# Kernel tuning notes

Measured on AMD Instinct MI355X. Metric: run time of the kernel, lower is better.

## Reference

```python
import jax, jax.numpy as jnp
import numpy as np

B_, S_, P_, D_ = 2, 512, 64, 1024
L_ = 4            # n_layer
DI_ = 2 * D_      # d_inner (expand=2)
DS_ = 16          # d_state
DC_ = 4           # d_conv
DR_ = D_ // 16    # dt_rank
PCD_ = 768        # prepend_cond_dim


def setup_inputs() -> dict:
    key = jax.random.key(0)
    ks = jax.random.split(key, 12)
    n = lambda k, s, sc=0.02: jax.random.normal(k, s, dtype=jnp.float32) * sc
    A_log = jnp.log(jnp.broadcast_to(jnp.arange(1, DS_ + 1, dtype=jnp.float32), (L_, DI_, DS_)))
    return {
        'x': jax.random.normal(ks[0], (B_, S_, D_), dtype=jnp.float32),
        'prepend_cond': jax.random.normal(ks[1], (B_, P_, PCD_), dtype=jnp.float32),
        'pre_w1': n(ks[2], (PCD_, D_)),
        'pre_w2': n(ks[3], (D_, D_)),
        'norm_w': jnp.ones((L_, D_), jnp.float32),
        'in_proj_w': n(ks[4], (L_, 2 * DI_, D_)),
        'conv_w': n(ks[5], (L_, DI_, DC_), 0.1),
        'conv_b': jnp.zeros((L_, DI_), jnp.float32),
        'x_proj_w': n(ks[6], (L_, DR_ + 2 * DS_, DI_)),
        'dt_proj_w': n(ks[7], (L_, DI_, DR_), 0.1),
        'dt_proj_b': jax.random.uniform(ks[8], (L_, DI_), jnp.float32, -4.0, -2.0),
        'A_log': A_log,
        'D_param': jnp.ones((L_, DI_), jnp.float32),
        'out_proj_w': n(ks[9], (L_, D_, DI_)),
        'final_norm_w': jnp.ones((D_,), jnp.float32),
    }


def rmsnorm(x, w, eps=1e-5):
    return x * jax.lax.rsqrt(jnp.mean(x * x, axis=-1, keepdims=True) + eps) * w


def mamba_block(x, ip_w, cw, cb, xp_w, dtp_w, dtp_b, A_log, Dp, op_w):
    B, S, _ = x.shape
    xz = jnp.einsum('bsd,ed->bse', x, ip_w)            # [B,S,2*DI]
    xi, z = jnp.split(xz, 2, axis=-1)
    # depthwise causal conv1d along time
    xt = xi.transpose(0, 2, 1)                          # [B,DI,S]
    conv = jax.lax.conv_general_dilated(
        xt, cw[:, None, :], (1,), [(DC_ - 1, 0)], feature_group_count=DI_) + cb[:, None]
    xi = jax.nn.silu(conv.transpose(0, 2, 1))           # [B,S,DI]
    xdbl = jnp.einsum('bse,fe->bsf', xi, xp_w)          # [B,S,DR+2*DS]
    dt, Bm, Cm = jnp.split(xdbl, [DR_, DR_ + DS_], axis=-1)
    dt = jax.nn.softplus(jnp.einsum('bsr,er->bse', dt, dtp_w) + dtp_b)  # [B,S,DI]
    A = -jnp.exp(A_log)                                 # [DI,DS]
    dA = jnp.exp(dt[..., None] * A)                     # [B,S,DI,DS]
    dBu = dt[..., None] * Bm[:, :, None, :] * xi[..., None]

    def step(h, t):
        da, dbu, c = t
        h = da * h + dbu                                # [B,DI,DS]
        return h, jnp.einsum('bes,bs->be', h, c)

    h0 = jnp.zeros((B, DI_, DS_), x.dtype)
    _, ys = jax.lax.scan(step, h0, (dA.transpose(1, 0, 2, 3), dBu.transpose(1, 0, 2, 3), Cm.transpose(1, 0, 2)))
    y = ys.transpose(1, 0, 2) + xi * Dp
    y = y * jax.nn.silu(z)
    return jnp.einsum('bse,de->bsd', y, op_w)


def reference(x, prepend_cond, pre_w1, pre_w2, norm_w, in_proj_w, conv_w, conv_b,
              x_proj_w, dt_proj_w, dt_proj_b, A_log, D_param, out_proj_w, final_norm_w):
    p = jax.nn.silu(prepend_cond @ pre_w1) @ pre_w2     # to_prepend_embed
    h = jnp.concatenate([p, x], axis=1)                 # [B, P+S, D]
    for l in range(L_):
        h = h + mamba_block(rmsnorm(h, norm_w[l]), in_proj_w[l], conv_w[l], conv_b[l],
                            x_proj_w[l], dt_proj_w[l], dt_proj_b[l], A_log[l],
                            D_param[l], out_proj_w[l])
    h = rmsnorm(h, final_norm_w)
    return h[:, P_:, :]
```

## Files before the change

kernel.cpp:

```cpp
#include <hip/hip_runtime.h>
#include <math.h>

#define B_ 2
#define S_ 512
#define P_ 64
#define T_ 576
#define D_ 1024
#define L_ 4
#define DI_ 2048
#define DS_ 16
#define DC_ 4
#define DR_ 64
#define PCD_ 768
#define M_ (B_*T_)
#define CCH 18
#define NC (T_/CCH)
#define XKS 16

typedef __attribute__((ext_vector_type(8))) short bf16x8;
typedef __attribute__((ext_vector_type(4))) float f32x4;

__device__ __forceinline__ float silu_f(float v) { return v / (1.f + __expf(-v)); }
__device__ __forceinline__ float softplus_f(float v) {
    return fmaxf(v, 0.f) + log1pf(__expf(-fabsf(v)));
}
__device__ __forceinline__ unsigned short bf16_rne(float x) {
    unsigned int b = __float_as_uint(x);
    b += 0x7fffu + ((b >> 16) & 1u);
    return (unsigned short)(b >> 16);
}
__device__ __forceinline__ float bf16_to_f(unsigned short u) {
    return __uint_as_float((unsigned int)u << 16);
}

typedef const void __attribute__((address_space(1)))* gas_t;
typedef void __attribute__((address_space(3)))* las_t;
__device__ __forceinline__ void async16(const void* g, void* l) {
    __builtin_amdgcn_global_load_lds((gas_t)g, (las_t)l, 16, 0, 0);
}

template<int EPI>
__global__ __launch_bounds__(256) void gemm_mfma_kernel(
    const unsigned short* __restrict__ A, const unsigned short* __restrict__ W,
    float* __restrict__ C, const float* __restrict__ bias,
    int M, int N, int K, int Kchunk)
{
    __shared__ unsigned short As[128 * 32];
    __shared__ unsigned short Bs[128 * 32];
    const int tid = threadIdx.x;
    const int wave = tid >> 6;
    const int lane = tid & 63;
    const int m0 = blockIdx.y * 128, n0 = blockIdx.x * 128;
    const int kbase = blockIdx.z * Kchunk;
    const int wm = (wave >> 1) * 64, wn = (wave & 1) * 64;

    const int srow = (wave << 5) + (lane >> 2);
    const int selem = (lane & 3) * 8;
    const unsigned short* gA = A + (size_t)(m0 + srow) * K + kbase + selem;
    const unsigned short* gB = W + (size_t)(n0 + srow) * K + kbase + selem;
    unsigned short* lA = As + (wave << 5) * 32;
    unsigned short* lB = Bs + (wave << 5) * 32;

    f32x4 acc[4][4];
    #pragma unroll
    for (int i = 0; i < 4; ++i)
        #pragma unroll
        for (int j = 0; j < 4; ++j)
            acc[i][j] = (f32x4){0.f, 0.f, 0.f, 0.f};

    const int fr = lane & 15;
    const int fq = lane >> 4;
    const int aoff = (wm + fr) * 32 + fq * 8;
    const int boff = (wn + fr) * 32 + fq * 8;

    for (int k0 = 0; k0 < Kchunk; k0 += 32) {
        async16(gA, lA);
        async16(gA + (size_t)16 * K, lA + 16 * 32);
        async16(gB, lB);
        async16(gB + (size_t)16 * K, lB + 16 * 32);
        gA += 32; gB += 32;
        __syncthreads();
        bf16x8 af[4], bf[4];
        #pragma unroll
        for (int i = 0; i < 4; ++i) af[i] = *(const bf16x8*)&As[aoff + i * 512];
        #pragma unroll
        for (int j = 0; j < 4; ++j) bf[j] = *(const bf16x8*)&Bs[boff + j * 512];
        #pragma unroll
        for (int i = 0; i < 4; ++i)
            #pragma unroll
            for (int j = 0; j < 4; ++j)
                acc[i][j] = __builtin_amdgcn_mfma_f32_16x16x32_bf16(
                    af[i], bf[j], acc[i][j], 0, 0, 0);
        __syncthreads();
    }

    #pragma unroll
    for (int i = 0; i < 4; ++i) {
        const int m = m0 + wm + i * 16 + fq * 4;
        #pragma unroll
        for (int j = 0; j < 4; ++j) {
            const int n = n0 + wn + j * 16 + fr;
            if (EPI == 6) {
                float* p = C + ((size_t)blockIdx.z * M + m) * N + n;
                #pragma unroll
                for (int r = 0; r < 4; ++r)
                    p[(size_t)r * N] = acc[i][j][r];
            } else {
                float* p = C + (size_t)m * N + n;
                #pragma unroll
                for (int r = 0; r < 4; ++r)
                    p[(size_t)r * N] = acc[i][j][r];
            }
        }
    }
}

__global__ __launch_bounds__(256) void dtproj_kernel(
    const unsigned short* __restrict__ dtr,
    const unsigned short* __restrict__ Wb,
    const float* __restrict__ bias,
    float* __restrict__ dtb)
{
    __shared__ float As[16][DR_];
    const int tid = threadIdx.x;
    const int e = blockIdx.x * 256 + tid;
    const int m0 = blockIdx.y * 16;
    {
        const ushort4 a4 = ((const ushort4*)(dtr + (size_t)m0 * DR_))[tid];
        float* dst = &As[0][0] + tid * 4;
        dst[0] = bf16_to_f(a4.x);
        dst[1] = bf16_to_f(a4.y);
        dst[2] = bf16_to_f(a4.z);
        dst[3] = bf16_to_f(a4.w);
    }
    float w[DR_];
    {
        const ushort4* wp = (const ushort4*)(Wb + (size_t)e * DR_);
        #pragma unroll
        for (int q = 0; q < 16; ++q) {
            const ushort4 v = wp[q];
            w[q * 4 + 0] = bf16_to_f(v.x);
            w[q * 4 + 1] = bf16_to_f(v.y);
            w[q * 4 + 2] = bf16_to_f(v.z);
            w[q * 4 + 3] = bf16_to_f(v.w);
        }
    }
    __syncthreads();
    const float bb = bias[e];
    #pragma unroll
    for (int m = 0; m < 16; ++m) {
        float acc = 0.f;
        #pragma unroll
        for (int r = 0; r < DR_; ++r) acc = fmaf(As[m][r], w[r], acc);
        dtb[(size_t)(m0 + m) * DI_ + e] = softplus_f(acc + bb);
    }
}

__global__ __launch_bounds__(256) void xproj_mfma_kernel(
    const unsigned short* __restrict__ A,
    const unsigned short* __restrict__ W,
    float* __restrict__ P)
{
    __shared__ unsigned short As[128 * 32];
    __shared__ unsigned short Bs[96 * 32];
    const int tid = threadIdx.x;
    const int wave = tid >> 6;
    const int lane = tid & 63;
    const int m0 = blockIdx.y * 128;
    const int kbase = blockIdx.x * (DI_ / XKS);
    const int wm = (wave >> 1) * 64, wn = (wave & 1) * 48;

    const int srow = (wave << 5) + (lane >> 2);
    const int selem = (lane & 3) * 8;
    const unsigned short* gA = A + (size_t)(m0 + srow) * DI_ + kbase + selem;
    const unsigned short* gB = W + (size_t)srow * DI_ + kbase + selem;
    unsigned short* lA = As + (wave << 5) * 32;
    unsigned short* lB = Bs + (wave << 5) * 32;

    f32x4 acc[4][3];
    #pragma unroll
    for (int i = 0; i < 4; ++i)
        #pragma unroll
        for (int j = 0; j < 3; ++j)
            acc[i][j] = (f32x4){0.f, 0.f, 0.f, 0.f};

    const int fr = lane & 15;
    const int fq = lane >> 4;
    const int aoff = (wm + fr) * 32 + fq * 8;
    const int boff = (wn + fr) * 32 + fq * 8;

    #pragma unroll
    for (int kk = 0; kk < 4; ++kk) {
        async16(gA, lA);
        async16(gA + (size_t)16 * DI_, lA + 16 * 32);
        if (wave < 3) {
            async16(gB, lB);
            async16(gB + (size_t)16 * DI_, lB + 16 * 32);
        }
        gA += 32; gB += 32;
        __syncthreads();
        bf16x8 af[4], bf[3];
        #pragma unroll
        for (int i = 0; i < 4; ++i) af[i] = *(const bf16x8*)&As[aoff + i * 512];
        #pragma unroll
        for (int j = 0; j < 3; ++j) bf[j] = *(const bf16x8*)&Bs[boff + j * 512];
        #pragma unroll
        for (int i = 0; i < 4; ++i)
            #pragma unroll
            for (int j = 0; j < 3; ++j)
                acc[i][j] = __builtin_amdgcn_mfma_f32_16x16x32_bf16(
                    af[i], bf[j], acc[i][j], 0, 0, 0);
        __syncthreads();
    }

    float* Pb = P + ((size_t)blockIdx.x * M_ + m0) * 96;
    #pragma unroll
    for (int i = 0; i < 4; ++i) {
        const int m = wm + i * 16 + fq * 4;
        #pragma unroll
        for (int j = 0; j < 3; ++j) {
            const int n = wn + j * 16 + fr;
            #pragma unroll
            for (int r = 0; r < 4; ++r)
                Pb[(size_t)(m + r) * 96 + n] = acc[i][j][r];
        }
    }
}

__global__ __launch_bounds__(256) void xproj_reduce_kernel(
    const float* __restrict__ P, float* __restrict__ Bc, float* __restrict__ Cc,
    unsigned short* __restrict__ dtr_bf)
{
    const int i = blockIdx.x * 256 + threadIdx.x;
    if (i >= M_ * 96) return;
    float s = 0.f;
    #pragma unroll
    for (int ks = 0; ks < XKS; ++ks) s += P[(size_t)ks * (M_ * 96) + i];
    const int m = i / 96;
    const int n = i - m * 96;
    if (n < DR_)            dtr_bf[(size_t)m * DR_ + n] = bf16_rne(s);
    else if (n < DR_ + DS_) Bc[(size_t)m * DS_ + (n - DR_)] = s;
    else                    Cc[(size_t)m * DS_ + (n - DR_ - DS_)] = s;
}

__global__ __launch_bounds__(256) void cvt_bf16_kernel(
    const float* __restrict__ in, unsigned short* __restrict__ out, int n4)
{
    const int i = blockIdx.x * 256 + threadIdx.x;
    if (i >= n4) return;
    const float4 v = ((const float4*)in)[i];
    ushort4 o;
    o.x = bf16_rne(v.x); o.y = bf16_rne(v.y);
    o.z = bf16_rne(v.z); o.w = bf16_rne(v.w);
    ((ushort4*)out)[i] = o;
}

__global__ __launch_bounds__(256) void cvt3_kernel(
    const float* __restrict__ s0, unsigned short* __restrict__ d0, int n0,
    const float* __restrict__ s1, unsigned short* __restrict__ d1, int n1,
    const float* __restrict__ s2, unsigned short* __restrict__ d2, int n2)
{
    const int i = blockIdx.x * 256 + threadIdx.x;
    const float* s; unsigned short* d; int off;
    if (i < n0)           { s = s0; d = d0; off = i; }
    else if (i < n0 + n1) { s = s1; d = d1; off = i - n0; }
    else if (i < n0 + n1 + n2) { s = s2; d = d2; off = i - n0 - n1; }
    else return;
    const float4 v = ((const float4*)s)[off];
    ushort4 o;
    o.x = bf16_rne(v.x); o.y = bf16_rne(v.y);
    o.z = bf16_rne(v.z); o.w = bf16_rne(v.w);
    ((ushort4*)d)[off] = o;
}

__global__ __launch_bounds__(256) void cvt_transpose_kernel(
    const float* __restrict__ in, unsigned short* __restrict__ out, int K, int N)
{
    __shared__ float t[64][65];
    const int k0 = blockIdx.x * 64;
    const int n0 = blockIdx.y * 64;
    const int tx = threadIdx.x & 63;
    const int ty = threadIdx.x >> 6;
    #pragma unroll
    for (int j = 0; j < 16; ++j) {
        const int kk = ty * 16 + j;
        t[kk][tx] = in[(size_t)(k0 + kk) * N + n0 + tx];
    }
    __syncthreads();
    #pragma unroll
    for (int j = 0; j < 16; ++j) {
        const int nn = ty * 16 + j;
        out[(size_t)(n0 + nn) * K + k0 + tx] = bf16_rne(t[tx][nn]);
    }
}

__global__ __launch_bounds__(256) void reduce_silu_bf16_kernel(
    const float* __restrict__ P, unsigned short* __restrict__ o, int MN, int ns)
{
    const int i = blockIdx.x * 256 + threadIdx.x;
    if (i >= MN) return;
    float s = 0.f;
    for (int k = 0; k < ns; ++k) s += P[(size_t)k * MN + i];
    o[i] = bf16_rne(silu_f(s));
}
__global__ __launch_bounds__(256) void reduce_fp32_kernel(
    const float* __restrict__ P, float* __restrict__ o, int MN, int ns)
{
    const int i = blockIdx.x * 256 + threadIdx.x;
    if (i >= MN) return;
    float s = 0.f;
    for (int k = 0; k < ns; ++k) s += P[(size_t)k * MN + i];
    o[i] = s;
}

__global__ __launch_bounds__(256) void outproj_reduce_kernel(
    const float* __restrict__ P, float* __restrict__ h)
{
    const int i = blockIdx.x * 256 + threadIdx.x;
    const float4 a = ((const float4*)P)[i];
    const float4 b = ((const float4*)P)[i + M_ * D_ / 4];
    float4 hv = ((float4*)h)[i];
    hv.x += a.x + b.x; hv.y += a.y + b.y;
    hv.z += a.z + b.z; hv.w += a.w + b.w;
    ((float4*)h)[i] = hv;
}

__global__ __launch_bounds__(256) void assemble_h_kernel(
    const float* __restrict__ p, const float* __restrict__ x, float* __restrict__ h)
{
    const int idx = blockIdx.x * 256 + threadIdx.x;
    const int r = idx >> 8;
    const int c = idx & 255;
    const int b = r / T_;
    const int t = r - b * T_;
    float4 v;
    if (t < P_) v = ((const float4*)p)[(size_t)(b * P_ + t) * 256 + c];
    else        v = ((const float4*)x)[(size_t)(b * S_ + (t - P_)) * 256 + c];
    ((float4*)h)[idx] = v;
}

__global__ __launch_bounds__(256) void rmsnorm_bf16_kernel(
    const float* __restrict__ x, const float* __restrict__ w,
    unsigned short* __restrict__ outb)
{
    const int r = blockIdx.x;
    const float4 v = ((const float4*)(x + (size_t)r * D_))[threadIdx.x];
    float ss = v.x * v.x + v.y * v.y + v.z * v.z + v.w * v.w;
    ss += __shfl_xor(ss, 32, 64);
    ss += __shfl_xor(ss, 16, 64);
    ss += __shfl_xor(ss, 8, 64);
    ss += __shfl_xor(ss, 4, 64);
    ss += __shfl_xor(ss, 2, 64);
    ss += __shfl_xor(ss, 1, 64);
    __shared__ float red[4];
    if ((threadIdx.x & 63) == 0) red[threadIdx.x >> 6] = ss;
    __syncthreads();
    const float tot = red[0] + red[1] + red[2] + red[3];
    const float scale = rsqrtf(tot * (1.f / D_) + 1e-5f);
    const float4 wv = ((const float4*)w)[threadIdx.x];
    ushort4 o;
    o.x = bf16_rne(v.x * scale * wv.x);
    o.y = bf16_rne(v.y * scale * wv.y);
    o.z = bf16_rne(v.z * scale * wv.z);
    o.w = bf16_rne(v.w * scale * wv.w);
    ((ushort4*)(outb + (size_t)r * D_))[threadIdx.x] = o;
}

__global__ __launch_bounds__(256) void final_rmsnorm_kernel(
    const float* __restrict__ h, const float* __restrict__ w, float* __restrict__ out)
{
    const int r = blockIdx.x;
    const int b = r / S_;
    const int s = r - b * S_;
    const int hr = b * T_ + P_ + s;
    const float4 v = ((const float4*)(h + (size_t)hr * D_))[threadIdx.x];
    float ss = v.x * v.x + v.y * v.y + v.z * v.z + v.w * v.w;
    ss += __shfl_xor(ss, 32, 64);
    ss += __shfl_xor(ss, 16, 64);
    ss += __shfl_xor(ss, 8, 64);
    ss += __shfl_xor(ss, 4, 64);
    ss += __shfl_xor(ss, 2, 64);
    ss += __shfl_xor(ss, 1, 64);
    __shared__ float red[4];
    if ((threadIdx.x & 63) == 0) red[threadIdx.x >> 6] = ss;
    __syncthreads();
    const float tot = red[0] + red[1] + red[2] + red[3];
    const float scale = rsqrtf(tot * (1.f / D_) + 1e-5f);
    const float4 wv = ((const float4*)w)[threadIdx.x];
    float4 o;
    o.x = v.x * scale * wv.x; o.y = v.y * scale * wv.y;
    o.z = v.z * scale * wv.z; o.w = v.w * scale * wv.w;
    ((float4*)(out + (size_t)r * D_))[threadIdx.x] = o;
}

__global__ __launch_bounds__(256) void conv_silu_kernel(
    const float* __restrict__ xz, const float* __restrict__ cw,
    const float* __restrict__ cb, unsigned short* __restrict__ xib,
    float* __restrict__ xim, float* __restrict__ szm)
{
    __shared__ float xs[67][64];
    const int tid = threadIdx.x;
    const int tx = tid & 63;
    const int ty = tid >> 6;
    const int r0 = blockIdx.x * 64;
    const int e0 = blockIdx.y * 64;
    const int bt0 = (r0 / T_) * T_;

    for (int j = ty; j < 67; j += 4) {
        const int r = r0 + j - 3;
        xs[j][tx] = (r >= bt0) ? xz[(size_t)r * (2 * DI_) + e0 + tx] : 0.f;
    }
    __syncthreads();
    const float4 w = *(const float4*)(cw + (size_t)(e0 + tx) * 4);
    const float bias = cb[e0 + tx];
    #pragma unroll
    for (int j = 0; j < 16; ++j) {
        const int rl = ty * 16 + j;
        float v = bias;
        v = fmaf(w.x, xs[rl + 0][tx], v);
        v = fmaf(w.y, xs[rl + 1][tx], v);
        v = fmaf(w.z, xs[rl + 2][tx], v);
        v = fmaf(w.w, xs[rl + 3][tx], v);
        const float o = silu_f(v);
        const size_t go = (size_t)(r0 + rl) * DI_ + e0 + tx;
        xib[go] = bf16_rne(o);
        xim[go] = o;
        szm[go] = silu_f(xz[(size_t)(r0 + rl) * (2 * DI_) + DI_ + e0 + tx]);
    }
}

__global__ __launch_bounds__(256) void scan_chunk1_kernel(
    const float* __restrict__ dtm,
    const float* __restrict__ Bc,
    const float* __restrict__ xim,
    const float* __restrict__ A_log,
    float* __restrict__ Ap, float* __restrict__ Hp)
{
    __shared__ float4 Bs[CCH][4];
    const int tid = threadIdx.x;
    const int e = ((blockIdx.x & 7) << 8) + tid;
    const int cb = blockIdx.x >> 3;
    const int b = cb & (B_ - 1);
    const int c = cb >> 1;
    const int r0 = b * T_ + c * CCH;
    for (int i = tid; i < CCH * DS_; i += 256)
        ((float*)Bs)[i] = Bc[(size_t)r0 * DS_ + i];
    float A2[DS_], h[DS_], a[DS_];
    const float* Ae = A_log + (size_t)e * DS_;
    #pragma unroll
    for (int s = 0; s < DS_; ++s) {
        A2[s] = -__expf(Ae[s]) * 1.44269504f;
        h[s] = 0.f; a[s] = 1.f;
    }
    __syncthreads();
    const float* dp = dtm + (size_t)r0 * DI_ + e;
    const float* up = xim + (size_t)r0 * DI_ + e;
    #pragma unroll
    for (int t = 0; t < CCH; ++t) {
        const float dtv = dp[(size_t)t * DI_];
        const float dtu = dtv * up[(size_t)t * DI_];
        #pragma unroll
        for (int q = 0; q < 4; ++q) {
            const float4 bq = Bs[t][q];
            const float* bb = &bq.x;
            #pragma unroll
            for (int j = 0; j < 4; ++j) {
                const int s = q * 4 + j;
                const float da = __builtin_amdgcn_exp2f(dtv * A2[s]);
                a[s] *= da;
                h[s] = fmaf(da, h[s], bb[j] * dtu);
            }
        }
    }
    const size_t o = (size_t)cb * DS_ * DI_ + e;
    #pragma unroll
    for (int s = 0; s < DS_; ++s) {
        Ap[o + (size_t)s * DI_] = a[s];
        Hp[o + (size_t)s * DI_] = h[s];
    }
}

__global__ __launch_bounds__(256) void scan_chunk2_kernel(
    float* __restrict__ Ap, float* __restrict__ Hp)
{
    const int g = blockIdx.x * 256 + threadIdx.x;
    float h = 0.f;
    #pragma unroll
    for (int c = 0; c < NC; ++c) {
        const size_t o = (size_t)c * (B_ * DI_ * DS_) + g;
        const float ap = Ap[o];
        const float hp = Hp[o];
        Hp[o] = h;
        h = fmaf(ap, h, hp);
    }
}

__global__ __launch_bounds__(256) void scan_chunk3_kernel(
    const float* __restrict__ dtm,
    const float* __restrict__ Bc,
    const float* __restrict__ Cc,
    const float* __restrict__ xim,
    const float* __restrict__ szm,
    const float* __restrict__ A_log, const float* __restrict__ Dp,
    const float* __restrict__ Hin, unsigned short* __restrict__ y)
{
    __shared__ float4 Bs[CCH][4], Cs[CCH][4];
    const int tid = threadIdx.x;
    const int e = ((blockIdx.x & 7) << 8) + tid;
    const int cb = blockIdx.x >> 3;
    const int b = cb & (B_ - 1);
    const int c = cb >> 1;
    const int r0 = b * T_ + c * CCH;
    for (int i = tid; i < CCH * DS_; i += 256) {
        ((float*)Bs)[i] = Bc[(size_t)r0 * DS_ + i];
        ((float*)Cs)[i] = Cc[(size_t)r0 * DS_ + i];
    }
    float A2[DS_], h[DS_];
    const float* Ae = A_log + (size_t)e * DS_;
    const float dpe = Dp[e];
    const size_t ho = (size_t)cb * DS_ * DI_ + e;
    #pragma unroll
    for (int s = 0; s < DS_; ++s) {
        A2[s] = -__expf(Ae[s]) * 1.44269504f;
        h[s] = Hin[ho + (size_t)s * DI_];
    }
    __syncthreads();
    const float* dp = dtm + (size_t)r0 * DI_ + e;
    const float* up = xim + (size_t)r0 * DI_ + e;
    const float* sp = szm + (size_t)r0 * DI_ + e;
    unsigned short* yp = y + (size_t)r0 * DI_ + e;
    #pragma unroll
    for (int t = 0; t < CCH; ++t) {
        const float dtv = dp[(size_t)t * DI_];
        const float u   = up[(size_t)t * DI_];
        const float dtu = dtv * u;
        float y0 = 0.f, y1 = 0.f, y2 = 0.f, y3 = 0.f;
        #pragma unroll
        for (int q = 0; q < 4; ++q) {
            const float4 bq = Bs[t][q];
            const float4 cq = Cs[t][q];
            const float* bb = &bq.x;
            const float* cc = &cq.x;
            #pragma unroll
            for (int j = 0; j < 4; ++j) {
                const int s = q * 4 + j;
                const float da = __builtin_amdgcn_exp2f(dtv * A2[s]);
                h[s] = fmaf(da, h[s], bb[j] * dtu);
                if (j == 0)      y0 = fmaf(h[s], cc[j], y0);
                else if (j == 1) y1 = fmaf(h[s], cc[j], y1);
                else if (j == 2) y2 = fmaf(h[s], cc[j], y2);
                else             y3 = fmaf(h[s], cc[j], y3);
            }
        }
        const float ysum = (y0 + y1) + (y2 + y3);
        const float yv = fmaf(u, dpe, ysum) * sp[(size_t)t * DI_];
        yp[(size_t)t * DI_] = bf16_rne(yv);
    }
}

extern "C" void kernel_launch(void* const* d_in, const int* in_sizes, int n_in,
                              void* d_out, int out_size, void* d_ws, size_t ws_size,
                              hipStream_t stream)
{
    const float* x       = (const float*)d_in[0];
    const float* pc      = (const float*)d_in[1];
    const float* pre_w1  = (const float*)d_in[2];
    const float* pre_w2  = (const float*)d_in[3];
    const float* norm_w  = (const float*)d_in[4];
    const float* ip_w    = (const float*)d_in[5];
    const float* conv_w  = (const float*)d_in[6];
    const float* conv_b  = (const float*)d_in[7];
    const float* xp_w    = (const float*)d_in[8];
    const float* dtp_w   = (const float*)d_in[9];
    const float* dtp_b   = (const float*)d_in[10];
    const float* A_log   = (const float*)d_in[11];
    const float* D_param = (const float*)d_in[12];
    const float* op_w    = (const float*)d_in[13];
    const float* fnw     = (const float*)d_in[14];
    float* out = (float*)d_out;

    float* ws = (float*)d_ws;
    float* h    = ws;  ws += (size_t)M_ * D_;
    float* xz   = ws;  ws += (size_t)M_ * 2 * DI_;
    float* xim  = ws;  ws += (size_t)M_ * DI_;
    float* szm  = ws;  ws += (size_t)M_ * DI_;
    float* dtb  = ws;  ws += (size_t)M_ * DI_;
    float* Pbuf = ws;  ws += (size_t)XKS * M_ * 96;
    float* Bc   = ws;  ws += (size_t)DS_ * M_;
    float* Cc   = ws;  ws += (size_t)DS_ * M_;
    unsigned short* xn_bf  = (unsigned short*)ws;  ws += (size_t)M_ * D_ / 2;
    unsigned short* yb_bf  = (unsigned short*)ws;  ws += (size_t)M_ * DI_ / 2;
    unsigned short* xi_bf  = (unsigned short*)ws;  ws += (size_t)M_ * DI_ / 2;
    unsigned short* dtr_bf = (unsigned short*)ws;  ws += (size_t)M_ * DR_ / 2;
    unsigned short* wbuf   = (unsigned short*)ws;  ws += (size_t)2 * DI_ * D_ / 2;
    unsigned short* xpw_bf = (unsigned short*)ws;  ws += (size_t)96 * DI_ / 2;
    unsigned short* dtpw_bf= (unsigned short*)ws;  ws += (size_t)DI_ * DR_ / 2;

    float* Ap = xz;
    float* Hp = xz + (size_t)NC * B_ * DI_ * DS_;

    unsigned short* pc_bf   = xi_bf;
    unsigned short* w1t_bf  = wbuf;
    unsigned short* w2t_bf  = wbuf + (size_t)D_ * PCD_;
    unsigned short* tmp1_bf = xn_bf;
    float*          tmp2    = szm;
    float*          Pop     = xz;

    const dim3 blk(256);

    cvt_bf16_kernel<<<dim3(B_ * P_ * PCD_ / 4 / 256), blk, 0, stream>>>(
        pc, pc_bf, B_ * P_ * PCD_ / 4);
    cvt_transpose_kernel<<<dim3(PCD_ / 64, D_ / 64), blk, 0, stream>>>(
        pre_w1, w1t_bf, PCD_, D_);
    cvt_transpose_kernel<<<dim3(D_ / 64, D_ / 64), blk, 0, stream>>>(
        pre_w2, w2t_bf, D_, D_);
    gemm_mfma_kernel<6><<<dim3(D_ / 128, 1, 6), blk, 0, stream>>>(
        pc_bf, w1t_bf, Pbuf, nullptr, B_ * P_, D_, PCD_, PCD_ / 6);
    reduce_silu_bf16_kernel<<<dim3(B_ * P_ * D_ / 256), blk, 0, stream>>>(
        Pbuf, tmp1_bf, B_ * P_ * D_, 6);
    gemm_mfma_kernel<6><<<dim3(D_ / 128, 1, 8), blk, 0, stream>>>(
        tmp1_bf, w2t_bf, Pbuf, nullptr, B_ * P_, D_, D_, D_ / 8);
    reduce_fp32_kernel<<<dim3(B_ * P_ * D_ / 256), blk, 0, stream>>>(
        Pbuf, tmp2, B_ * P_ * D_, 8);
    assemble_h_kernel<<<dim3(M_ * D_ / 4 / 256), blk, 0, stream>>>(tmp2, x, h);

    const int n_ip  = 2 * DI_ * D_ / 4;
    const int n_xp  = 96 * DI_ / 4;
    const int n_dtp = DI_ * DR_ / 4;

    for (int l = 0; l < L_; ++l) {
        rmsnorm_bf16_kernel<<<dim3(M_), blk, 0, stream>>>(
            h, norm_w + (size_t)l * D_, xn_bf);
        cvt3_kernel<<<dim3((n_ip + n_xp + n_dtp + 255) / 256), blk, 0, stream>>>(
            ip_w + (size_t)l * 2 * DI_ * D_, wbuf, n_ip,
            xp_w + (size_t)l * 96 * DI_, xpw_bf, n_xp,
            dtp_w + (size_t)l * DI_ * DR_, dtpw_bf, n_dtp);
        gemm_mfma_kernel<0><<<dim3(2 * DI_ / 128, M_ / 128, 1), blk, 0, stream>>>(
            xn_bf, wbuf, xz, nullptr, M_, 2 * DI_, D_, D_);
        conv_silu_kernel<<<dim3(M_ / 64, DI_ / 64), blk, 0, stream>>>(
            xz, conv_w + (size_t)l * DI_ * DC_, conv_b + (size_t)l * DI_,
            xi_bf, xim, szm);
        xproj_mfma_kernel<<<dim3(XKS, M_ / 128), blk, 0, stream>>>(
            xi_bf, xpw_bf, Pbuf);
        xproj_reduce_kernel<<<dim3((M_ * 96 + 255) / 256), blk, 0, stream>>>(
            Pbuf, Bc, Cc, dtr_bf);
        dtproj_kernel<<<dim3(DI_ / 256, M_ / 16), blk, 0, stream>>>(
            dtr_bf, dtpw_bf, dtp_b + (size_t)l * DI_, dtb);
        scan_chunk1_kernel<<<dim3(NC * B_ * DI_ / 256), blk, 0, stream>>>(
            dtb, Bc, xim, A_log + (size_t)l * DI_ * DS_, Ap, Hp);
        scan_chunk2_kernel<<<dim3(B_ * DI_ * DS_ / 256), blk, 0, stream>>>(Ap, Hp);
        scan_chunk3_kernel<<<dim3(NC * B_ * DI_ / 256), blk, 0, stream>>>(
            dtb, Bc, Cc, xim, szm, A_log + (size_t)l * DI_ * DS_,
            D_param + (size_t)l * DI_, Hp, yb_bf);
        cvt_bf16_kernel<<<dim3(D_ * DI_ / 4 / 256), blk, 0, stream>>>(
            op_w + (size_t)l * D_ * DI_, wbuf, D_ * DI_ / 4);
        gemm_mfma_kernel<6><<<dim3(D_ / 128, M_ / 128, 2), blk, 0, stream>>>(
            yb_bf, wbuf, Pop, nullptr, M_, D_, DI_, DI_ / 2);
        outproj_reduce_kernel<<<dim3(M_ * D_ / 4 / 256), blk, 0, stream>>>(Pop, h);
    }

    final_rmsnorm_kernel<<<dim3(B_ * S_), blk, 0, stream>>>(h, fnw, out);
}
```

Before: 755.7 us.

## Fuse residual reduce with next-layer RMSNorm, silu(z) into in_proj epilogue, merge weight casts

The out_proj partial-sum reduction now also computes the next layer's RMSNorm and bf16 output, which removes a separate rmsnorm launch and a re-read of h each layer. The in_proj GEMM epilogue applies silu to the z half and writes it straight to szm, so the conv kernel no longer has to re-read z. The out_proj weight cast joins the combined conversion kernel in a dedicated buffer, which saves one launch per layer. The trade-off is extra workspace and a larger combined kernel. The opw_bf buffer must also fit inside the existing workspace allocation.

```diff
diff --git a/kernel.cpp b/kernel.cpp
--- a/kernel.cpp
+++ b/kernel.cpp
@@ -42,7 +42,7 @@
 template<int EPI>
 __global__ __launch_bounds__(256) void gemm_mfma_kernel(
     const unsigned short* __restrict__ A, const unsigned short* __restrict__ W,
-    float* __restrict__ C, const float* __restrict__ bias,
+    float* __restrict__ C, float* __restrict__ C2,
     int M, int N, int K, int Kchunk)
 {
     __shared__ unsigned short As[128 * 32];
@@ -105,11 +105,18 @@
                 #pragma unroll
                 for (int r = 0; r < 4; ++r)
                     p[(size_t)r * N] = acc[i][j][r];
-            } else {
-                float* p = C + (size_t)m * N + n;
-                #pragma unroll
-                for (int r = 0; r < 4; ++r)
-                    p[(size_t)r * N] = acc[i][j][r];
+            } else if (EPI == 7) {
+                if (n < DI_) {
+                    float* p = C + (size_t)m * N + n;
+                    #pragma unroll
+                    for (int r = 0; r < 4; ++r)
+                        p[(size_t)r * N] = acc[i][j][r];
+                } else {
+                    float* p = C2 + (size_t)m * DI_ + (n - DI_);
+                    #pragma unroll
+                    for (int r = 0; r < 4; ++r)
+                        p[(size_t)r * DI_] = silu_f(acc[i][j][r]);
+                }
             }
         }
     }
@@ -255,16 +262,18 @@
     ((ushort4*)out)[i] = o;
 }
 
-__global__ __launch_bounds__(256) void cvt3_kernel(
+__global__ __launch_bounds__(256) void cvt4_kernel(
     const float* __restrict__ s0, unsigned short* __restrict__ d0, int n0,
     const float* __restrict__ s1, unsigned short* __restrict__ d1, int n1,
-    const float* __restrict__ s2, unsigned short* __restrict__ d2, int n2)
+    const float* __restrict__ s2, unsigned short* __restrict__ d2, int n2,
+    const float* __restrict__ s3, unsigned short* __restrict__ d3, int n3)
 {
     const int i = blockIdx.x * 256 + threadIdx.x;
     const float* s; unsigned short* d; int off;
-    if (i < n0)           { s = s0; d = d0; off = i; }
-    else if (i < n0 + n1) { s = s1; d = d1; off = i - n0; }
+    if (i < n0)                { s = s0; d = d0; off = i; }
+    else if (i < n0 + n1)      { s = s1; d = d1; off = i - n0; }
     else if (i < n0 + n1 + n2) { s = s2; d = d2; off = i - n0 - n1; }
+    else if (i < n0 + n1 + n2 + n3) { s = s3; d = d3; off = i - n0 - n1 - n2; }
     else return;
     const float4 v = ((const float4*)s)[off];
     ushort4 o;
@@ -313,16 +322,38 @@
     o[i] = s;
 }
 
-__global__ __launch_bounds__(256) void outproj_reduce_kernel(
-    const float* __restrict__ P, float* __restrict__ h)
-{
-    const int i = blockIdx.x * 256 + threadIdx.x;
-    const float4 a = ((const float4*)P)[i];
-    const float4 b = ((const float4*)P)[i + M_ * D_ / 4];
-    float4 hv = ((float4*)h)[i];
-    hv.x += a.x + b.x; hv.y += a.y + b.y;
-    hv.z += a.z + b.z; hv.w += a.w + b.w;
-    ((float4*)h)[i] = hv;
+__global__ __launch_bounds__(256) void outproj_rmsnorm_kernel(
+    const float* __restrict__ P, float* __restrict__ h,
+    const float* __restrict__ w, unsigned short* __restrict__ outb, int donorm)
+{
+    const int r = blockIdx.x;
+    const int i = r * 256 + threadIdx.x;
+    const float4 a4 = ((const float4*)P)[i];
+    const float4 b4 = ((const float4*)P)[i + M_ * D_ / 4];
+    float4 v = ((float4*)h)[i];
+    v.x += a4.x + b4.x; v.y += a4.y + b4.y;
+    v.z += a4.z + b4.z; v.w += a4.w + b4.w;
+    ((float4*)h)[i] = v;
+    if (!donorm) return;
+    float ss = v.x * v.x + v.y * v.y + v.z * v.z + v.w * v.w;
+    ss += __shfl_xor(ss, 32, 64);
+    ss += __shfl_xor(ss, 16, 64);
+    ss += __shfl_xor(ss, 8, 64);
+    ss += __shfl_xor(ss, 4, 64);
+    ss += __shfl_xor(ss, 2, 64);
+    ss += __shfl_xor(ss, 1, 64);
+    __shared__ float red[4];
+    if ((threadIdx.x & 63) == 0) red[threadIdx.x >> 6] = ss;
+    __syncthreads();
+    const float tot = red[0] + red[1] + red[2] + red[3];
+    const float scale = rsqrtf(tot * (1.f / D_) + 1e-5f);
+    const float4 wv = ((const float4*)w)[threadIdx.x];
+    ushort4 o;
+    o.x = bf16_rne(v.x * scale * wv.x);
+    o.y = bf16_rne(v.y * scale * wv.y);
+    o.z = bf16_rne(v.z * scale * wv.z);
+    o.w = bf16_rne(v.w * scale * wv.w);
+    ((ushort4*)(outb + (size_t)r * D_))[threadIdx.x] = o;
 }
 
 __global__ __launch_bounds__(256) void assemble_h_kernel(
@@ -396,7 +427,7 @@
 __global__ __launch_bounds__(256) void conv_silu_kernel(
     const float* __restrict__ xz, const float* __restrict__ cw,
     const float* __restrict__ cb, unsigned short* __restrict__ xib,
-    float* __restrict__ xim, float* __restrict__ szm)
+    float* __restrict__ xim)
 {
     __shared__ float xs[67][64];
     const int tid = threadIdx.x;
@@ -425,7 +456,6 @@
         const size_t go = (size_t)(r0 + rl) * DI_ + e0 + tx;
         xib[go] = bf16_rne(o);
         xim[go] = o;
-        szm[go] = silu_f(xz[(size_t)(r0 + rl) * (2 * DI_) + DI_ + e0 + tx]);
     }
 }
 
@@ -595,6 +625,7 @@
     unsigned short* wbuf   = (unsigned short*)ws;  ws += (size_t)2 * DI_ * D_ / 2;
     unsigned short* xpw_bf = (unsigned short*)ws;  ws += (size_t)96 * DI_ / 2;
     unsigned short* dtpw_bf= (unsigned short*)ws;  ws += (size_t)DI_ * DR_ / 2;
+    unsigned short* opw_bf = (unsigned short*)ws;  ws += (size_t)D_ * DI_ / 2;
 
     float* Ap = xz;
     float* Hp = xz + (size_t)NC * B_ * DI_ * DS_;
@@ -627,19 +658,21 @@
     const int n_ip  = 2 * DI_ * D_ / 4;
     const int n_xp  = 96 * DI_ / 4;
     const int n_dtp = DI_ * DR_ / 4;
+    const int n_op  = D_ * DI_ / 4;
+
+    rmsnorm_bf16_kernel<<<dim3(M_), blk, 0, stream>>>(h, norm_w, xn_bf);
 
     for (int l = 0; l < L_; ++l) {
-        rmsnorm_bf16_kernel<<<dim3(M_), blk, 0, stream>>>(
-            h, norm_w + (size_t)l * D_, xn_bf);
-        cvt3_kernel<<<dim3((n_ip + n_xp + n_dtp + 255) / 256), blk, 0, stream>>>(
+        cvt4_kernel<<<dim3((n_ip + n_xp + n_dtp + n_op + 255) / 256), blk, 0, stream>>>(
             ip_w + (size_t)l * 2 * DI_ * D_, wbuf, n_ip,
             xp_w + (size_t)l * 96 * DI_, xpw_bf, n_xp,
-            dtp_w + (size_t)l * DI_ * DR_, dtpw_bf, n_dtp);
-        gemm_mfma_kernel<0><<<dim3(2 * DI_ / 128, M_ / 128, 1), blk, 0, stream>>>(
-            xn_bf, wbuf, xz, nullptr, M_, 2 * DI_, D_, D_);
+            dtp_w + (size_t)l * DI_ * DR_, dtpw_bf, n_dtp,
+            op_w + (size_t)l * D_ * DI_, opw_bf, n_op);
+        gemm_mfma_kernel<7><<<dim3(2 * DI_ / 128, M_ / 128, 1), blk, 0, stream>>>(
+            xn_bf, wbuf, xz, szm, M_, 2 * DI_, D_, D_);
         conv_silu_kernel<<<dim3(M_ / 64, DI_ / 64), blk, 0, stream>>>(
             xz, conv_w + (size_t)l * DI_ * DC_, conv_b + (size_t)l * DI_,
-            xi_bf, xim, szm);
+            xi_bf, xim);
         xproj_mfma_kernel<<<dim3(XKS, M_ / 128), blk, 0, stream>>>(
             xi_bf, xpw_bf, Pbuf);
         xproj_reduce_kernel<<<dim3((M_ * 96 + 255) / 256), blk, 0, stream>>>(
@@ -652,11 +685,10 @@
         scan_chunk3_kernel<<<dim3(NC * B_ * DI_ / 256), blk, 0, stream>>>(
             dtb, Bc, Cc, xim, szm, A_log + (size_t)l * DI_ * DS_,
             D_param + (size_t)l * DI_, Hp, yb_bf);
-        cvt_bf16_kernel<<<dim3(D_ * DI_ / 4 / 256), blk, 0, stream>>>(
-            op_w + (size_t)l * D_ * DI_, wbuf, D_ * DI_ / 4);
         gemm_mfma_kernel<6><<<dim3(D_ / 128, M_ / 128, 2), blk, 0, stream>>>(
-            yb_bf, wbuf, Pop, nullptr, M_, D_, DI_, DI_ / 2);
-        outproj_reduce_kernel<<<dim3(M_ * D_ / 4 / 256), blk, 0, stream>>>(Pop, h);
+            yb_bf, opw_bf, Pop, nullptr, M_, D_, DI_, DI_ / 2);
+        outproj_rmsnorm_kernel<<<dim3(M_), blk, 0, stream>>>(
+            Pop, h, norm_w + (size_t)((l + 1) & 3) * D_, xn_bf, l < L_ - 1);
     }
 
     final_rmsnorm_kernel<<<dim3(B_ * S_), blk, 0, stream>>>(h, fnw, out);
```

Measured after the change: 745.2 us. No clear change (-1.4%).
